# Performance work log

Measured on AMD Instinct MI355X. Metric: run time of the kernel, lower is better.

Reference implementation:

```python
import jax, jax.numpy as jnp
import numpy as np

N = 100_000      # nodes
E = 1_600_000    # edges (before self-loops)
IN = 128         # in_channels
HID = 32         # hidden_channels
HEADS = 2        # attention heads
OUT = 64         # out_channels
NEG_SLOPE = 0.2  # PyG GATConv leaky-relu slope


def setup_inputs() -> dict:
    key = jax.random.key(0)
    ks = jax.random.split(key, 16)
    HC = HID * HEADS

    def glorot(k, shape, fan_in):
        return jax.random.normal(k, shape, jnp.float32) / np.sqrt(fan_in)

    return {
        "x": jax.random.normal(ks[0], (N, IN), jnp.float32),
        "edge_index": jax.random.randint(ks[1], (2, E), 0, N, jnp.int64),
        # layer 1: IN -> HID per head, concat
        "W1": glorot(ks[2], (IN, HC), IN),
        "as1": glorot(ks[3], (HEADS, HID), HID),
        "ad1": glorot(ks[4], (HEADS, HID), HID),
        "b1": jnp.zeros((HC,), jnp.float32),
        # layer 2: HC -> HID per head, concat
        "W2": glorot(ks[5], (HC, HC), HC),
        "as2": glorot(ks[6], (HEADS, HID), HID),
        "ad2": glorot(ks[7], (HEADS, HID), HID),
        "b2": jnp.zeros((HC,), jnp.float32),
        # layer 3: HC -> OUT, 1 head, no concat
        "W3": glorot(ks[8], (HC, OUT), HC),
        "as3": glorot(ks[9], (1, OUT), OUT),
        "ad3": glorot(ks[10], (1, OUT), OUT),
        "b3": jnp.zeros((OUT,), jnp.float32),
    }


def gat_conv(x, src, dst, W, a_src, a_dst, b, heads, out_ch, concat, n):
    # per-head linear transform: [n, heads, out_ch]
    h = (x @ W).reshape(n, heads, out_ch)
    # per-node attention logits: [n, heads]
    al_src = jnp.einsum('nhc,hc->nh', h, a_src)
    al_dst = jnp.einsum('nhc,hc->nh', h, a_dst)
    # raw edge scores with leaky relu: [e, heads]
    e = al_src[src] + al_dst[dst]
    e = jnp.where(e >= 0, e, NEG_SLOPE * e)
    # segment softmax over incoming edges of each dst node
    m = jax.ops.segment_max(e, dst, num_segments=n)          # [n, heads]
    ee = jnp.exp(e - m[dst])
    denom = jax.ops.segment_sum(ee, dst, num_segments=n)     # [n, heads]
    alpha = ee / denom[dst]
    # weighted scatter-add of source features
    out = jax.ops.segment_sum(h[src] * alpha[..., None], dst, num_segments=n)
    if concat:
        out = out.reshape(n, heads * out_ch)
    else:
        out = out.mean(axis=1)
    return out + b


def reference(x, edge_index, W1, as1, ad1, b1, W2, as2, ad2, b2, W3, as3, ad3, b3):
    # PyG GATConv adds self-loops by default
    loop = jnp.arange(N, dtype=edge_index.dtype)
    src = jnp.concatenate([edge_index[0], loop])
    dst = jnp.concatenate([edge_index[1], loop])

    h = gat_conv(x, src, dst, W1, as1, ad1, b1, HEADS, HID, True, N)
    h = jax.nn.relu(h)
    h = gat_conv(h, src, dst, W2, as2, ad2, b2, HEADS, HID, True, N)
    h = jax.nn.relu(h)
    out = gat_conv(h, src, dst, W3, as3, ad3, b3, 1, OUT, False, N)
    return out
```

## Files before the change

kernel.cpp:

```cpp
#include <hip/hip_runtime.h>
#include <hip/hip_fp16.h>

#define IN_CH   128
#define HC      64
#define NEG_SLOPE 0.2f

#define BSH   9
#define NPB   512
#define EPB   8192

typedef __attribute__((ext_vector_type(8))) _Float16 f16x8;
typedef __attribute__((ext_vector_type(4))) float    f32x4;

__global__ __launch_bounds__(256) void scan1_k(const int* __restrict__ deg, int* __restrict__ tmp,
                                               int* __restrict__ bsum, int n) {
    __shared__ int s[256];
    int tid = threadIdx.x;
    int i = blockIdx.x * 256 + tid;
    int v = (i < n) ? deg[i] : 0;
    s[tid] = v; __syncthreads();
    for (int o = 1; o < 256; o <<= 1) {
        int t = (tid >= o) ? s[tid - o] : 0;
        __syncthreads();
        s[tid] += t;
        __syncthreads();
    }
    if (i < n) tmp[i] = s[tid] - v;
    if (tid == 255) bsum[blockIdx.x] = s[255];
}

__global__ __launch_bounds__(512) void scan2_k(int* __restrict__ bsum, int nb) {
    __shared__ int s[512];
    int tid = threadIdx.x;
    int v = (tid < nb) ? bsum[tid] : 0;
    s[tid] = v; __syncthreads();
    for (int o = 1; o < 512; o <<= 1) {
        int t = (tid >= o) ? s[tid - o] : 0;
        __syncthreads();
        s[tid] += t;
        __syncthreads();
    }
    if (tid < nb) bsum[tid] = s[tid] - v;
}

__global__ __launch_bounds__(256) void combine_k(const int* __restrict__ tmp, const int* __restrict__ bsum,
                                                 int* __restrict__ base, int n) {
    int i = blockIdx.x * 256 + threadIdx.x;
    if (i < n) base[i] = tmp[i] + bsum[blockIdx.x];
}

__global__ __launch_bounds__(256) void csortA1_k(const int* __restrict__ ei, int* __restrict__ countsT,
                                                 int E, int nbuck, int neb) {
    __shared__ int cnt[256];
    cnt[threadIdx.x] = 0;
    __syncthreads();
    int base = blockIdx.x * EPB;
#pragma unroll
    for (int k = 0; k < EPB / 256; k++) {
        int i = base + k * 256 + threadIdx.x;
        if (i < E) atomicAdd(&cnt[ei[E + i] >> BSH], 1);
    }
    __syncthreads();
    if (threadIdx.x < nbuck) countsT[threadIdx.x * neb + blockIdx.x] = cnt[threadIdx.x];
}

__global__ __launch_bounds__(256) void csortA3_k(const int* __restrict__ ei, const int* __restrict__ baseT,
                                                 unsigned* __restrict__ pairs, int E, int nbuck, int neb) {
    __shared__ int cur[256];
    if (threadIdx.x < nbuck) cur[threadIdx.x] = baseT[threadIdx.x * neb + blockIdx.x];
    __syncthreads();
    int base = blockIdx.x * EPB;
#pragma unroll
    for (int k = 0; k < EPB / 256; k++) {
        int i = base + k * 256 + threadIdx.x;
        if (i < E) {
            int d = ei[E + i];
            int s = ei[i];
            int p = atomicAdd(&cur[d >> BSH], 1);
            pairs[p] = ((unsigned)(d & (NPB - 1)) << 17) | (unsigned)s;
        }
    }
}

__global__ __launch_bounds__(256) void csortB2_k(const unsigned* __restrict__ pairs, const int* __restrict__ baseT,
                                                 int* __restrict__ off, int* __restrict__ csr,
                                                 int N, int E, int nbuck, int neb) {
    __shared__ int cnt[NPB];
    __shared__ int cur[NPB];
    __shared__ int ps[256];
    int b = blockIdx.x;
    int tid = threadIdx.x;
    int rs = baseT[b * neb];
    int re = (b + 1 < nbuck) ? baseT[(b + 1) * neb] : E;

    cnt[tid] = 0; cnt[tid + 256] = 0;
    __syncthreads();
    for (int j = rs + tid; j < re; j += 256)
        atomicAdd(&cnt[pairs[j] >> 17], 1);
    __syncthreads();

    int c0 = cnt[2 * tid], c1 = cnt[2 * tid + 1];
    int pair = c0 + c1;
    ps[tid] = pair;
    __syncthreads();
    for (int o = 1; o < 256; o <<= 1) {
        int t = (tid >= o) ? ps[tid - o] : 0;
        __syncthreads();
        ps[tid] += t;
        __syncthreads();
    }
    int base0 = rs + ps[tid] - pair;
    int n0 = b * NPB + 2 * tid;
    cur[2 * tid] = base0;
    cur[2 * tid + 1] = base0 + c0;
    if (n0 < N)     off[n0] = base0;
    if (n0 + 1 < N) off[n0 + 1] = base0 + c0;
    if (b == nbuck - 1 && tid == 0) off[N] = E;
    if (b == nbuck - 1 && tid < 8) csr[E + tid] = 0;
    __syncthreads();

    for (int j = rs + tid; j < re; j += 256) {
        unsigned v = pairs[j];
        int p = atomicAdd(&cur[v >> 17], 1);
        csr[p] = (int)(v & 0x1FFFF);
    }
}

__global__ __launch_bounds__(256) void wpack_k(const float* __restrict__ W, _Float16* __restrict__ P, int total) {
    int o = blockIdx.x * 256 + threadIdx.x;
    if (o >= total) return;
    int j = o & 7, l = (o >> 3) & 63, t = (o >> 9) & 3, s = o >> 11;
    int row = s * 32 + ((l >> 4) << 3) + j;
    int col = (t << 4) + (l & 15);
    P[o] = (_Float16)W[row * 64 + col];
}

template<int K, int HEADS>
__global__ __launch_bounds__(256) void gemm_mfma_k(const float* __restrict__ X, const _Float16* __restrict__ P,
                                                   const float* __restrict__ a_s, const float* __restrict__ a_d,
                                                   __half* __restrict__ H, float* __restrict__ ALS,
                                                   float* __restrict__ ALD, int n) {
    __shared__ _Float16 lh[4][16 * 72];
    int tid = threadIdx.x;
    int wv = tid >> 6, lane = tid & 63;
    int wid = blockIdx.x * 4 + wv;
    int rowbase = wid << 4;
    if (rowbase >= n) return;
    int q = lane >> 4, cl = lane & 15;

    f16x8 b[K / 32][4];
    const f16x8* Pv = (const f16x8*)P;
#pragma unroll
    for (int s = 0; s < K / 32; s++)
#pragma unroll
        for (int t = 0; t < 4; t++)
            b[s][t] = Pv[(s * 4 + t) * 64 + lane];

    f32x4 c[4];
#pragma unroll
    for (int t = 0; t < 4; t++) c[t] = (f32x4){0.f, 0.f, 0.f, 0.f};

    const float* xrow = X + (size_t)(rowbase + cl) * K + q * 8;
#pragma unroll
    for (int s = 0; s < K / 32; s++) {
        float4 x0 = *(const float4*)(xrow + s * 32);
        float4 x1 = *(const float4*)(xrow + s * 32 + 4);
        f16x8 a;
        a[0] = (_Float16)x0.x; a[1] = (_Float16)x0.y; a[2] = (_Float16)x0.z; a[3] = (_Float16)x0.w;
        a[4] = (_Float16)x1.x; a[5] = (_Float16)x1.y; a[6] = (_Float16)x1.z; a[7] = (_Float16)x1.w;
#pragma unroll
        for (int t = 0; t < 4; t++)
            c[t] = __builtin_amdgcn_mfma_f32_16x16x32_f16(a, b[s][t], c[t], 0, 0, 0);
    }

    if (HEADS == 2) {
        float as0 = a_s[cl], as1 = a_s[16 + cl], as2 = a_s[32 + cl], as3 = a_s[48 + cl];
        float ad0 = a_d[cl], ad1 = a_d[16 + cl], ad2 = a_d[32 + cl], ad3 = a_d[48 + cl];
#pragma unroll
        for (int reg = 0; reg < 4; reg++) {
            float s0 = c[0][reg] * as0 + c[1][reg] * as1;
            float d0 = c[0][reg] * ad0 + c[1][reg] * ad1;
            float s1 = c[2][reg] * as2 + c[3][reg] * as3;
            float d1 = c[2][reg] * ad2 + c[3][reg] * ad3;
#pragma unroll
            for (int m = 1; m <= 8; m <<= 1) {
                s0 += __shfl_xor(s0, m, 64);
                d0 += __shfl_xor(d0, m, 64);
                s1 += __shfl_xor(s1, m, 64);
                d1 += __shfl_xor(d1, m, 64);
            }
            if (cl == 0) {
                int row = rowbase + q * 4 + reg;
                ALS[row * 2]     = s0;
                ALS[row * 2 + 1] = s1;
                ALD[row * 2]     = d0;
                ALD[row * 2 + 1] = d1;
            }
        }
    } else {
        float as0 = a_s[cl], as1 = a_s[16 + cl], as2 = a_s[32 + cl], as3 = a_s[48 + cl];
        float ad0 = a_d[cl], ad1 = a_d[16 + cl], ad2 = a_d[32 + cl], ad3 = a_d[48 + cl];
#pragma unroll
        for (int reg = 0; reg < 4; reg++) {
            float s0 = c[0][reg] * as0 + c[1][reg] * as1 + c[2][reg] * as2 + c[3][reg] * as3;
            float d0 = c[0][reg] * ad0 + c[1][reg] * ad1 + c[2][reg] * ad2 + c[3][reg] * ad3;
#pragma unroll
            for (int m = 1; m <= 8; m <<= 1) {
                s0 += __shfl_xor(s0, m, 64);
                d0 += __shfl_xor(d0, m, 64);
            }
            if (cl == 0) {
                int row = rowbase + q * 4 + reg;
                ALS[row] = s0;
                ALD[row] = d0;
            }
        }
    }

    _Float16* L = lh[wv];
#pragma unroll
    for (int t = 0; t < 4; t++)
#pragma unroll
        for (int reg = 0; reg < 4; reg++)
            L[(q * 4 + reg) * 72 + t * 16 + cl] = (_Float16)c[t][reg];
    __builtin_amdgcn_s_waitcnt(0);
    int rr = lane >> 2, seg = lane & 3;
    uint4 v0 = *(const uint4*)((const char*)L + rr * 144 + seg * 32);
    uint4 v1 = *(const uint4*)((const char*)L + rr * 144 + seg * 32 + 16);
    char* hb = (char*)(H + (size_t)rowbase * 64);
    *(uint4*)(hb + rr * 128 + seg * 32)      = v0;
    *(uint4*)(hb + rr * 128 + seg * 32 + 16) = v1;
}

template<int HEADS, int RELU>
__global__ __launch_bounds__(256) void aggregate_k(const __half* __restrict__ H, const float* __restrict__ ALS,
                                                   const float* __restrict__ ALD, const int* __restrict__ off,
                                                   const int* __restrict__ csr, const float* __restrict__ bias,
                                                   float* __restrict__ OUT, int n) {
    int lane = threadIdx.x & 63;
    int wv   = threadIdx.x >> 6;
    int c2   = lane & 31;
    int dst  = blockIdx.x * 8 + wv * 2 + (lane >> 5);
    bool alive = dst < n;
    int dsafe = alive ? dst : 0;
    int head = (HEADS == 2) ? (c2 >> 4) : 0;

    int b0 = off[dsafe];
    int b1 = alive ? off[dsafe + 1] : b0;
    float ald = ALD[dsafe * HEADS + head];

    float e = ALS[dsafe * HEADS + head] + ald;
    e = fmaxf(e, NEG_SLOPE * e);
    float ee = alive ? __expf(e) : 0.f;
    float den = ee;
    const __half2* Hc = (const __half2*)H;
    float2 hs = __half22float2(Hc[dsafe * 32 + c2]);
    float accx = ee * hs.x, accy = ee * hs.y;

    int len = b1 - b0;
    int lmax = max(len, __shfl_xor(len, 32, 64));

    int j = 0;
    for (; j + 7 < lmax; j += 8) {
        int i0 = b0 + j;
        int s[8];
#pragma unroll
        for (int k = 0; k < 8; k++) s[k] = csr[i0 + k];
        float al[8];
#pragma unroll
        for (int k = 0; k < 8; k++) al[k] = ALS[s[k] * HEADS + head];
        float2 h[8];
#pragma unroll
        for (int k = 0; k < 8; k++) h[k] = __half22float2(Hc[s[k] * 32 + c2]);
#pragma unroll
        for (int k = 0; k < 8; k++) {
            float ek = al[k] + ald;
            ek = fmaxf(ek, NEG_SLOPE * ek);
            float wk = (j + k < len) ? __expf(ek) : 0.f;
            den += wk;
            accx += wk * h[k].x;
            accy += wk * h[k].y;
        }
    }
    for (; j < lmax; j++) {
        int s0 = csr[b0 + j];
        float a0 = ALS[s0 * HEADS + head];
        float2 h0 = __half22float2(Hc[s0 * 32 + c2]);
        float e0 = a0 + ald;
        e0 = fmaxf(e0, NEG_SLOPE * e0);
        float w0 = (j < len) ? __expf(e0) : 0.f;
        den += w0;
        accx += w0 * h0.x;
        accy += w0 * h0.y;
    }

    if (alive) {
        float2 bi = ((const float2*)bias)[c2];
        float rd = 1.f / den;
        float ox = accx * rd + bi.x;
        float oy = accy * rd + bi.y;
        if (RELU) {
            ox = (ox > 0.f) ? ox : 0.f;
            oy = (oy > 0.f) ? oy : 0.f;
        }
        ((float2*)OUT)[dst * 32 + c2] = make_float2(ox, oy);
    }
}

extern "C" void kernel_launch(void* const* d_in, const int* in_sizes, int n_in,
                              void* d_out, int out_size, void* d_ws, size_t ws_size,
                              hipStream_t stream) {
    const float* x   = (const float*)d_in[0];
    const int*   ei  = (const int*)  d_in[1];
    const float* W1  = (const float*)d_in[2];
    const float* as1 = (const float*)d_in[3];
    const float* ad1 = (const float*)d_in[4];
    const float* b1  = (const float*)d_in[5];
    const float* W2  = (const float*)d_in[6];
    const float* as2 = (const float*)d_in[7];
    const float* ad2 = (const float*)d_in[8];
    const float* b2  = (const float*)d_in[9];
    const float* W3  = (const float*)d_in[10];
    const float* as3 = (const float*)d_in[11];
    const float* ad3 = (const float*)d_in[12];
    const float* b3  = (const float*)d_in[13];

    const int N = in_sizes[0] / IN_CH;
    const int E = in_sizes[1] / 2;
    const int NBUCK = (N + NPB - 1) >> BSH;
    const int NEB   = (E + EPB - 1) / EPB;
    const int NT    = NBUCK * NEB;

    char* p = (char*)d_ws;
    auto carve = [&](size_t bytes) {
        char* r = p;
        p += (bytes + 255) & ~(size_t)255;
        return r;
    };
    __half*    hbuf    = (__half*)   carve((size_t)N * HC * 2);
    float*     obuf    = (float*)    carve((size_t)N * HC * 4);
    float*     als     = (float*)    carve((size_t)N * 2 * 4);
    float*     ald     = (float*)    carve((size_t)N * 2 * 4);
    int*       off     = (int*)      carve((size_t)(N + 1) * 4);
    int*       tmp     = (int*)      carve((size_t)NT * 4);
    int*       bsum    = (int*)      carve((size_t)((NT + 255) / 256 + 1) * 4);
    int*       csr     = (int*)      carve((size_t)(E + 8) * 4);
    unsigned*  pairs   = (unsigned*) carve((size_t)E * 4);
    int*       countsT = (int*)      carve((size_t)NT * 4);
    int*       baseT   = (int*)      carve((size_t)NT * 4);
    _Float16*  wp1     = (_Float16*) carve((size_t)IN_CH * 64 * 2);
    _Float16*  wp2     = (_Float16*) carve((size_t)64 * 64 * 2);
    _Float16*  wp3     = (_Float16*) carve((size_t)64 * 64 * 2);

    const int NTB = (NT + 255) / 256;
    const int NW2 = (N + 7) / 8;
    const int NBM = (N / 16 + 3) / 4;

    wpack_k<<<(IN_CH * 64) / 256, 256, 0, stream>>>(W1, wp1, IN_CH * 64);
    wpack_k<<<(64 * 64) / 256, 256, 0, stream>>>(W2, wp2, 64 * 64);
    wpack_k<<<(64 * 64) / 256, 256, 0, stream>>>(W3, wp3, 64 * 64);

    csortA1_k<<<NEB, 256, 0, stream>>>(ei, countsT, E, NBUCK, NEB);
    scan1_k  <<<NTB, 256, 0, stream>>>(countsT, tmp, bsum, NT);
    scan2_k  <<<1, 512, 0, stream>>>(bsum, NTB);
    combine_k<<<NTB, 256, 0, stream>>>(tmp, bsum, baseT, NT);
    csortA3_k<<<NEB, 256, 0, stream>>>(ei, baseT, pairs, E, NBUCK, NEB);
    csortB2_k<<<NBUCK, 256, 0, stream>>>(pairs, baseT, off, csr, N, E, NBUCK, NEB);

    gemm_mfma_k<128, 2><<<NBM, 256, 0, stream>>>(x, wp1, as1, ad1, hbuf, als, ald, N);
    aggregate_k<2, 1>  <<<NW2, 256, 0, stream>>>(hbuf, als, ald, off, csr, b1, obuf, N);

    gemm_mfma_k<64, 2><<<NBM, 256, 0, stream>>>(obuf, wp2, as2, ad2, hbuf, als, ald, N);
    aggregate_k<2, 1> <<<NW2, 256, 0, stream>>>(hbuf, als, ald, off, csr, b2, obuf, N);

    gemm_mfma_k<64, 1><<<NBM, 256, 0, stream>>>(obuf, wp3, as3, ad3, hbuf, als, ald, N);
    aggregate_k<1, 0> <<<NW2, 256, 0, stream>>>(hbuf, als, ald, off, csr, b3, (float*)d_out, N);
}
```

Before: 349.8 us.

## Sort destination nodes by degree and pack four nodes per wavefront in aggregation

Adds a counting sort of destination nodes by in-degree (histogram, scan, rank kernels) to build a permutation, so nodes sharing a wavefront have similar edge counts and less lane divergence from the max-length loop. The aggregation kernel now handles four destinations per wave with 16 lanes each, loading 8-byte half4 feature chunks and writing float4 outputs. The csr padding grows to 64 entries. This adds five small preprocessing launches, and permuted destination order gives less regular output writes.

```diff
diff --git a/kernel.cpp b/kernel.cpp
--- a/kernel.cpp
+++ b/kernel.cpp
@@ -8,6 +8,7 @@
 #define BSH   9
 #define NPB   512
 #define EPB   8192
+#define DBIN  64
 
 typedef __attribute__((ext_vector_type(8))) _Float16 f16x8;
 typedef __attribute__((ext_vector_type(4))) float    f32x4;
@@ -116,13 +117,40 @@
     if (n0 < N)     off[n0] = base0;
     if (n0 + 1 < N) off[n0 + 1] = base0 + c0;
     if (b == nbuck - 1 && tid == 0) off[N] = E;
-    if (b == nbuck - 1 && tid < 8) csr[E + tid] = 0;
+    if (b == nbuck - 1 && tid < 64) csr[E + tid] = 0;
     __syncthreads();
 
     for (int j = rs + tid; j < re; j += 256) {
         unsigned v = pairs[j];
         int p = atomicAdd(&cur[v >> 17], 1);
         csr[p] = (int)(v & 0x1FFFF);
+    }
+}
+
+__global__ __launch_bounds__(256) void dhist_k(const int* __restrict__ off, int* __restrict__ countsD,
+                                               int N, int nb) {
+    __shared__ int cnt[DBIN];
+    if (threadIdx.x < DBIN) cnt[threadIdx.x] = 0;
+    __syncthreads();
+    int i = blockIdx.x * 256 + threadIdx.x;
+    if (i < N) {
+        int d = min(off[i + 1] - off[i], DBIN - 1);
+        atomicAdd(&cnt[d], 1);
+    }
+    __syncthreads();
+    if (threadIdx.x < DBIN) countsD[threadIdx.x * nb + blockIdx.x] = cnt[threadIdx.x];
+}
+
+__global__ __launch_bounds__(256) void drank_k(const int* __restrict__ off, const int* __restrict__ baseD,
+                                               int* __restrict__ perm, int N, int nb) {
+    __shared__ int cur[DBIN];
+    if (threadIdx.x < DBIN) cur[threadIdx.x] = baseD[threadIdx.x * nb + blockIdx.x];
+    __syncthreads();
+    int i = blockIdx.x * 256 + threadIdx.x;
+    if (i < N) {
+        int d = min(off[i + 1] - off[i], DBIN - 1);
+        int p = atomicAdd(&cur[d], 1);
+        perm[p] = i;
     }
 }
 
@@ -235,30 +263,32 @@
 template<int HEADS, int RELU>
 __global__ __launch_bounds__(256) void aggregate_k(const __half* __restrict__ H, const float* __restrict__ ALS,
                                                    const float* __restrict__ ALD, const int* __restrict__ off,
-                                                   const int* __restrict__ csr, const float* __restrict__ bias,
-                                                   float* __restrict__ OUT, int n) {
+                                                   const int* __restrict__ csr, const int* __restrict__ perm,
+                                                   const float* __restrict__ bias, float* __restrict__ OUT, int n) {
     int lane = threadIdx.x & 63;
     int wv   = threadIdx.x >> 6;
-    int c2   = lane & 31;
-    int dst  = blockIdx.x * 8 + wv * 2 + (lane >> 5);
-    bool alive = dst < n;
-    int dsafe = alive ? dst : 0;
-    int head = (HEADS == 2) ? (c2 >> 4) : 0;
-
-    int b0 = off[dsafe];
-    int b1 = alive ? off[dsafe + 1] : b0;
-    float ald = ALD[dsafe * HEADS + head];
-
-    float e = ALS[dsafe * HEADS + head] + ald;
+    int c4   = lane & 15;
+    int idx  = blockIdx.x * 16 + wv * 4 + (lane >> 4);
+    bool alive = idx < n;
+    int dst = perm[alive ? idx : 0];
+    int head = (HEADS == 2) ? (c4 >> 3) : 0;
+
+    int b0 = off[dst];
+    int len = alive ? (off[dst + 1] - b0) : 0;
+    float ald = ALD[dst * HEADS + head];
+
+    float e = ALS[dst * HEADS + head] + ald;
     e = fmaxf(e, NEG_SLOPE * e);
     float ee = alive ? __expf(e) : 0.f;
     float den = ee;
-    const __half2* Hc = (const __half2*)H;
-    float2 hs = __half22float2(Hc[dsafe * 32 + c2]);
-    float accx = ee * hs.x, accy = ee * hs.y;
-
-    int len = b1 - b0;
-    int lmax = max(len, __shfl_xor(len, 32, 64));
+    const uint2* Hq = (const uint2*)H;
+    uint2 hv = Hq[dst * 16 + c4];
+    float2 hl = __half22float2(*(const __half2*)&hv.x);
+    float2 hh = __half22float2(*(const __half2*)&hv.y);
+    float a0 = ee * hl.x, a1 = ee * hl.y, a2 = ee * hh.x, a3 = ee * hh.y;
+
+    int lmax = max(len, __shfl_xor(len, 16, 64));
+    lmax = max(lmax, __shfl_xor(lmax, 32, 64));
 
     int j = 0;
     for (; j + 7 < lmax; j += 8) {
@@ -269,41 +299,47 @@
         float al[8];
 #pragma unroll
         for (int k = 0; k < 8; k++) al[k] = ALS[s[k] * HEADS + head];
-        float2 h[8];
-#pragma unroll
-        for (int k = 0; k < 8; k++) h[k] = __half22float2(Hc[s[k] * 32 + c2]);
+        uint2 h[8];
+#pragma unroll
+        for (int k = 0; k < 8; k++) h[k] = Hq[s[k] * 16 + c4];
 #pragma unroll
         for (int k = 0; k < 8; k++) {
             float ek = al[k] + ald;
             ek = fmaxf(ek, NEG_SLOPE * ek);
             float wk = (j + k < len) ? __expf(ek) : 0.f;
+            float2 l2 = __half22float2(*(const __half2*)&h[k].x);
+            float2 h2 = __half22float2(*(const __half2*)&h[k].y);
             den += wk;
-            accx += wk * h[k].x;
-            accy += wk * h[k].y;
+            a0 += wk * l2.x; a1 += wk * l2.y;
+            a2 += wk * h2.x; a3 += wk * h2.y;
         }
     }
     for (; j < lmax; j++) {
         int s0 = csr[b0 + j];
-        float a0 = ALS[s0 * HEADS + head];
-        float2 h0 = __half22float2(Hc[s0 * 32 + c2]);
-        float e0 = a0 + ald;
+        float alv = ALS[s0 * HEADS + head];
+        uint2 h0 = Hq[s0 * 16 + c4];
+        float e0 = alv + ald;
         e0 = fmaxf(e0, NEG_SLOPE * e0);
         float w0 = (j < len) ? __expf(e0) : 0.f;
+        float2 l2 = __half22float2(*(const __half2*)&h0.x);
+        float2 h2 = __half22float2(*(const __half2*)&h0.y);
         den += w0;
-        accx += w0 * h0.x;
-        accy += w0 * h0.y;
+        a0 += w0 * l2.x; a1 += w0 * l2.y;
+        a2 += w0 * h2.x; a3 += w0 * h2.y;
     }
 
     if (alive) {
-        float2 bi = ((const float2*)bias)[c2];
+        float4 bi = ((const float4*)bias)[c4];
         float rd = 1.f / den;
-        float ox = accx * rd + bi.x;
-        float oy = accy * rd + bi.y;
+        float o0 = a0 * rd + bi.x;
+        float o1 = a1 * rd + bi.y;
+        float o2 = a2 * rd + bi.z;
+        float o3 = a3 * rd + bi.w;
         if (RELU) {
-            ox = (ox > 0.f) ? ox : 0.f;
-            oy = (oy > 0.f) ? oy : 0.f;
+            o0 = fmaxf(o0, 0.f); o1 = fmaxf(o1, 0.f);
+            o2 = fmaxf(o2, 0.f); o3 = fmaxf(o3, 0.f);
         }
-        ((float2*)OUT)[dst * 32 + c2] = make_float2(ox, oy);
+        ((float4*)OUT)[dst * 16 + c4] = make_float4(o0, o1, o2, o3);
     }
 }
 
@@ -330,6 +366,8 @@
     const int NBUCK = (N + NPB - 1) >> BSH;
     const int NEB   = (E + EPB - 1) / EPB;
     const int NT    = NBUCK * NEB;
+    const int NB    = (N + 255) / 256;
+    const int ND    = DBIN * NB;
 
     char* p = (char*)d_ws;
     auto carve = [&](size_t bytes) {
@@ -344,16 +382,20 @@
     int*       off     = (int*)      carve((size_t)(N + 1) * 4);
     int*       tmp     = (int*)      carve((size_t)NT * 4);
     int*       bsum    = (int*)      carve((size_t)((NT + 255) / 256 + 1) * 4);
-    int*       csr     = (int*)      carve((size_t)(E + 8) * 4);
+    int*       csr     = (int*)      carve((size_t)(E + 64) * 4);
     unsigned*  pairs   = (unsigned*) carve((size_t)E * 4);
     int*       countsT = (int*)      carve((size_t)NT * 4);
     int*       baseT   = (int*)      carve((size_t)NT * 4);
+    int*       countsD = (int*)      carve((size_t)ND * 4);
+    int*       baseD   = (int*)      carve((size_t)ND * 4);
+    int*       perm    = (int*)      carve((size_t)N * 4);
     _Float16*  wp1     = (_Float16*) carve((size_t)IN_CH * 64 * 2);
     _Float16*  wp2     = (_Float16*) carve((size_t)64 * 64 * 2);
     _Float16*  wp3     = (_Float16*) carve((size_t)64 * 64 * 2);
 
     const int NTB = (NT + 255) / 256;
-    const int NW2 = (N + 7) / 8;
+    const int NDB = (ND + 255) / 256;
+    const int NW4 = (N + 15) / 16;
     const int NBM = (N / 16 + 3) / 4;
 
     wpack_k<<<(IN_CH * 64) / 256, 256, 0, stream>>>(W1, wp1, IN_CH * 64);
@@ -367,12 +409,18 @@
     csortA3_k<<<NEB, 256, 0, stream>>>(ei, baseT, pairs, E, NBUCK, NEB);
     csortB2_k<<<NBUCK, 256, 0, stream>>>(pairs, baseT, off, csr, N, E, NBUCK, NEB);
 
+    dhist_k  <<<NB, 256, 0, stream>>>(off, countsD, N, NB);
+    scan1_k  <<<NDB, 256, 0, stream>>>(countsD, tmp, bsum, ND);
+    scan2_k  <<<1, 512, 0, stream>>>(bsum, NDB);
+    combine_k<<<NDB, 256, 0, stream>>>(tmp, bsum, baseD, ND);
+    drank_k  <<<NB, 256, 0, stream>>>(off, baseD, perm, N, NB);
+
     gemm_mfma_k<128, 2><<<NBM, 256, 0, stream>>>(x, wp1, as1, ad1, hbuf, als, ald, N);
-    aggregate_k<2, 1>  <<<NW2, 256, 0, stream>>>(hbuf, als, ald, off, csr, b1, obuf, N);
+    aggregate_k<2, 1>  <<<NW4, 256, 0, stream>>>(hbuf, als, ald, off, csr, perm, b1, obuf, N);
 
     gemm_mfma_k<64, 2><<<NBM, 256, 0, stream>>>(obuf, wp2, as2, ad2, hbuf, als, ald, N);
-    aggregate_k<2, 1> <<<NW2, 256, 0, stream>>>(hbuf, als, ald, off, csr, b2, obuf, N);
+    aggregate_k<2, 1> <<<NW4, 256, 0, stream>>>(hbuf, als, ald, off, csr, perm, b2, obuf, N);
 
     gemm_mfma_k<64, 1><<<NBM, 256, 0, stream>>>(obuf, wp3, as3, ad3, hbuf, als, ald, N);
-    aggregate_k<1, 0> <<<NW2, 256, 0, stream>>>(hbuf, als, ald, off, csr, b3, (float*)d_out, N);
-}
+    aggregate_k<1, 0> <<<NW4, 256, 0, stream>>>(hbuf, als, ald, off, csr, perm, b3, (float*)d_out, N);
+}
```

Result: faster. 334.8 us (-4.3%).
